# Kernel optimization log

Measured on AMD Instinct MI355X. Metric: run time of the kernel, lower is better.

Reference implementation:

```python
import jax, jax.numpy as jnp
import numpy as np

OUT, IN = 8192, 8192
GROUP = 128
N_GROUPS = IN // GROUP
BATCH = 64


def dequant_int4(packed, scales):
    # packed: [OUT, IN//2] int32 bytes in [0,256); two 4-bit codes per byte
    low = packed & 0xF            # first element of each pair
    high = (packed >> 4) & 0xF    # second element
    q = jnp.stack([low, high], axis=-1).reshape(OUT, IN)  # interleaved nibbles
    # symmetric grouped dequant: w = (q - 8) * scale, scale per [row, group]
    qg = q.reshape(OUT, N_GROUPS, GROUP).astype(scales.dtype)
    w = (qg - 8.0) * scales[:, :, None]
    return w.reshape(OUT, IN)


def setup_inputs() -> dict:
    key = jax.random.key(0)
    k1, k2, k3 = jax.random.split(key, 3)
    x = jax.random.normal(k1, (BATCH, IN), dtype=jnp.float32)
    packed = jax.random.randint(k2, (OUT, IN // 2), 0, 256, dtype=jnp.int32)
    scales = jax.random.uniform(k3, (OUT, N_GROUPS), dtype=jnp.float32)
    return {"x": x, "packed": packed, "scales": scales}


def reference(x, packed, scales):
    # Dequantize int4 weights then dense matmul (F.linear, no bias)
    w = dequant_int4(packed, scales)        # [OUT, IN]
    return jnp.einsum('bi,oi->bo', x, w)    # [BATCH, OUT]
```

## Files before the change

kernel.cpp:

```cpp
#include <hip/hip_runtime.h>
#include <hip/hip_bf16.h>
#include <stdint.h>

#define OUTN   8192
#define INN    8192
#define NGRP   64
#define BATCHN 64
#define BN     64
#define BK     64
#define KSPLIT 8
#define KCHUNK (INN / KSPLIT)
#define NITER  (KCHUNK / BK)
#define NGRPC  (KCHUNK / 128)
#define OSZ    (BATCHN * OUTN)

typedef __attribute__((ext_vector_type(8))) short bf16x8;
typedef __attribute__((ext_vector_type(8))) unsigned short u16x8;
typedef __attribute__((ext_vector_type(4))) float f32x4;
typedef __attribute__((ext_vector_type(4))) unsigned int u32x4;

__device__ __forceinline__ unsigned short f2bf(float f) {
  __hip_bfloat16 h = __float2bfloat16(f);
  return __builtin_bit_cast(unsigned short, h);
}
__device__ __forceinline__ float bf2f(unsigned short h) {
  unsigned int u = ((unsigned int)h) << 16;
  return __builtin_bit_cast(float, u);
}

__device__ __forceinline__ void gll16(const void* g, void* l) {
  __builtin_amdgcn_global_load_lds(
      (const __attribute__((address_space(1))) unsigned int*)g,
      (__attribute__((address_space(3))) unsigned int*)l, 16, 0, 0);
}

__global__ void qlin_prep(const float* __restrict__ x, float* __restrict__ xsum,
                          unsigned short* __restrict__ xbf) {
  const int b = blockIdx.x;
  const int t = threadIdx.x;
  const float* xrow = x + (size_t)b * INN + t * 32;
  unsigned short* orow = xbf + (size_t)b * INN + t * 32;
  float s = 0.0f;
#pragma unroll
  for (int c = 0; c < 4; ++c) {
    float4 v0 = *(const float4*)(xrow + c * 8);
    float4 v1 = *(const float4*)(xrow + c * 8 + 4);
    u16x8 h;
    h[0] = f2bf(v0.x); h[1] = f2bf(v0.y); h[2] = f2bf(v0.z); h[3] = f2bf(v0.w);
    h[4] = f2bf(v1.x); h[5] = f2bf(v1.y); h[6] = f2bf(v1.z); h[7] = f2bf(v1.w);
#pragma unroll
    for (int j = 0; j < 8; ++j) s += bf2f(h[j]);
    *(u16x8*)(orow + c * 8) = h;
  }
  __shared__ float parts[256];
  parts[t] = s;
  __syncthreads();
  if (t < NGRP) {
    float g = parts[4 * t] + parts[4 * t + 1] + parts[4 * t + 2] + parts[4 * t + 3];
    xsum[t * BATCHN + b] = g;
  }
}

__global__ __launch_bounds__(256, 4) void qlin_main(
    const int* __restrict__ packed, const unsigned short* __restrict__ xbf,
    const float* __restrict__ scales, const float* __restrict__ xsum,
    float* __restrict__ out, float* __restrict__ part) {
  const int bx    = blockIdx.x;
  const int ks    = bx & (KSPLIT - 1);
  const int ntile = bx >> 3;
  const int o0    = ntile * BN;
  const int g0    = ks * NGRPC;

  const int t    = threadIdx.x;
  const int lane = t & 63;
  const int w    = t >> 6;
  const int l15  = lane & 15;
  const int quad = lane >> 4;

  __shared__ __align__(16) int4  pkb[3][512];
  __shared__ __align__(16) int4  xb[3][512];
  __shared__ __align__(16) float st[BN][9];
  __shared__ __align__(16) float xs[NGRPC][BATCHN];

#pragma unroll
  for (int i = 0; i < 2; ++i) {
    int v = t * 2 + i;
    int ol = v >> 3, gl = v & 7;
    st[ol][gl] = scales[(size_t)(o0 + ol) * NGRP + g0 + gl];
    int gl2 = v >> 6, b2 = v & 63;
    xs[gl2][b2] = xsum[(g0 + gl2) * BATCHN + b2];
  }

  const int row0 = t >> 3;
  const int p0   = t & 7;
  const int c0   = p0 ^ (row0 & 7);
  const char* pk0 = (const char*)packed + (size_t)(o0 + row0) * 16384 + ks * 2048 + c0 * 16;
  const char* pk1 = pk0 + (size_t)32 * 16384;
  const char* xg0 = (const char*)xbf + (size_t)row0 * 16384 + ks * 2048 + c0 * 16;
  const char* xg1 = xg0 + (size_t)32 * 16384;

  auto issue = [&](int i, int buf) {
    const size_t off = (size_t)i * 128;
    gll16(pk0 + off, &pkb[buf][t]);
    gll16(pk1 + off, &pkb[buf][256 + t]);
    gll16(xg0 + off, &xb[buf][t]);
    gll16(xg1 + off, &xb[buf][256 + t]);
  };

  f32x4 facc[4], gacc[4];
#pragma unroll
  for (int mt = 0; mt < 4; ++mt) {
    facc[mt] = (f32x4){0.f, 0.f, 0.f, 0.f};
    gacc[mt] = (f32x4){0.f, 0.f, 0.f, 0.f};
  }

  issue(0, 0);
  issue(1, 1);

  const int browB = w * 16 + l15;
  const int sw    = l15 & 7;

#pragma unroll
  for (int i = 0; i < NITER; ++i) {
    if (i == 0)
      asm volatile("s_waitcnt vmcnt(4) lgkmcnt(0)" ::: "memory");
    else if (i == NITER - 1)
      asm volatile("s_waitcnt vmcnt(0)" ::: "memory");
    else
      asm volatile("s_waitcnt vmcnt(4)" ::: "memory");
    __builtin_amdgcn_sched_barrier(0);
    __builtin_amdgcn_s_barrier();
    __builtin_amdgcn_sched_barrier(0);

    if (i + 2 < NITER) issue(i + 2, (i + 2) % 3);

    const int cur = i % 3;
#pragma unroll
    for (int kq = 0; kq < 2; ++kq) {
      const int ch = kq * 4 + quad;
      int4 v = pkb[cur][browB * 8 + (ch ^ sw)];
      u32x4 bw;
      bw.x = 0x43004300u | ((unsigned)v.x & 0xFu) | (((unsigned)v.x & 0xF0u) << 12);
      bw.y = 0x43004300u | ((unsigned)v.y & 0xFu) | (((unsigned)v.y & 0xF0u) << 12);
      bw.z = 0x43004300u | ((unsigned)v.z & 0xFu) | (((unsigned)v.z & 0xF0u) << 12);
      bw.w = 0x43004300u | ((unsigned)v.w & 0xFu) | (((unsigned)v.w & 0xF0u) << 12);
      bf16x8 bfv = __builtin_bit_cast(bf16x8, bw);
#pragma unroll
      for (int mt = 0; mt < 4; ++mt) {
        bf16x8 af = *(const bf16x8*)&xb[cur][(mt * 16 + l15) * 8 + (ch ^ sw)];
        gacc[mt] = __builtin_amdgcn_mfma_f32_16x16x32_bf16(af, bfv, gacc[mt], 0, 0, 0);
      }
    }

    if (i & 1) {
      const int g = i >> 1;
      float s0 = st[browB][g];
#pragma unroll
      for (int mt = 0; mt < 4; ++mt) {
        f32x4 xv = *(const f32x4*)&xs[g][mt * 16 + quad * 4];
#pragma unroll
        for (int r = 0; r < 4; ++r) {
          facc[mt][r] += s0 * (gacc[mt][r] - 136.0f * xv[r]);
          gacc[mt][r] = 0.f;
        }
      }
    }
  }

  const int obase = o0 + browB;
  if (part) {
    float* pb = part + (size_t)ks * OSZ;
#pragma unroll
    for (int mt = 0; mt < 4; ++mt)
#pragma unroll
      for (int r = 0; r < 4; ++r) {
        int m = mt * 16 + quad * 4 + r;
        pb[(size_t)m * OUTN + obase] = facc[mt][r];
      }
  } else {
#pragma unroll
    for (int mt = 0; mt < 4; ++mt)
#pragma unroll
      for (int r = 0; r < 4; ++r) {
        int m = mt * 16 + quad * 4 + r;
        atomicAdd(&out[(size_t)m * OUTN + obase], facc[mt][r]);
      }
  }
}

__global__ void qlin_reduce(const float* __restrict__ part, float* __restrict__ out) {
  const size_t i = ((size_t)blockIdx.x * 256 + threadIdx.x) * 4;
  float4 s = *(const float4*)(part + i);
#pragma unroll
  for (int ks = 1; ks < KSPLIT; ++ks) {
    float4 v = *(const float4*)(part + (size_t)ks * OSZ + i);
    s.x += v.x; s.y += v.y; s.z += v.z; s.w += v.w;
  }
  *(float4*)(out + i) = s;
}

extern "C" void kernel_launch(void* const* d_in, const int* in_sizes, int n_in,
                              void* d_out, int out_size, void* d_ws, size_t ws_size,
                              hipStream_t stream) {
  const float* x      = (const float*)d_in[0];
  const int*   packed = (const int*)d_in[1];
  const float* scales = (const float*)d_in[2];
  float* out  = (float*)d_out;

  float*          xsum = (float*)d_ws;
  unsigned short* xbf  = (unsigned short*)((char*)d_ws + 16384);
  const size_t part_off = 16384 + (size_t)BATCHN * INN * 2;
  const size_t need = part_off + (size_t)KSPLIT * OSZ * sizeof(float);
  float* part = (ws_size >= need) ? (float*)((char*)d_ws + part_off) : nullptr;

  qlin_prep<<<BATCHN, 256, 0, stream>>>(x, xsum, xbf);
  if (!part)
    hipMemsetAsync(d_out, 0, (size_t)out_size * sizeof(float), stream);
  qlin_main<<<(OUTN / BN) * KSPLIT, 256, 0, stream>>>(packed, xbf, scales, xsum, out, part);
  if (part)
    qlin_reduce<<<OSZ / 4 / 256, 256, 0, stream>>>(part, out);
}
```

Baseline: 212.3 us.

## Load packed weights directly into registers instead of staging through LDS

Packed int4 weight tiles are now fetched by each lane straight from global memory into registers, double-buffered as even and odd register sets one iteration ahead. They no longer go through global_load_lds into a triple-buffered LDS array. This drops the LDS write and read traffic for weights, along with their bank-swizzle lookups, and frees 24KB of shared memory. The cost is more registers, only one iteration of prefetch distance for the weights, and vmcnt accounting that now mixes direct vector loads with the LDS-bound x loads.

```diff
diff --git a/kernel.cpp b/kernel.cpp
--- a/kernel.cpp
+++ b/kernel.cpp
@@ -77,7 +77,6 @@
   const int l15  = lane & 15;
   const int quad = lane >> 4;
 
-  __shared__ __align__(16) int4  pkb[3][512];
   __shared__ __align__(16) int4  xb[3][512];
   __shared__ __align__(16) float st[BN][9];
   __shared__ __align__(16) float xs[NGRPC][BATCHN];
@@ -91,22 +90,25 @@
     xs[gl2][b2] = xsum[(g0 + gl2) * BATCHN + b2];
   }
 
+  const int browB = w * 16 + l15;
+  const int sw    = l15 & 7;
+
   const int row0 = t >> 3;
-  const int p0   = t & 7;
-  const int c0   = p0 ^ (row0 & 7);
-  const char* pk0 = (const char*)packed + (size_t)(o0 + row0) * 16384 + ks * 2048 + c0 * 16;
-  const char* pk1 = pk0 + (size_t)32 * 16384;
+  const int c0   = (t & 7) ^ (row0 & 7);
   const char* xg0 = (const char*)xbf + (size_t)row0 * 16384 + ks * 2048 + c0 * 16;
   const char* xg1 = xg0 + (size_t)32 * 16384;
 
-  auto issue = [&](int i, int buf) {
+  auto issueG = [&](int i, int buf) {
     const size_t off = (size_t)i * 128;
-    gll16(pk0 + off, &pkb[buf][t]);
-    gll16(pk1 + off, &pkb[buf][256 + t]);
     gll16(xg0 + off, &xb[buf][t]);
     gll16(xg1 + off, &xb[buf][256 + t]);
   };
 
+  const char* pkL = (const char*)packed + (size_t)(o0 + browB) * 16384 +
+                    ks * 2048 + quad * 16;
+
+  int4 pkE[2], pkO[2];
+
   f32x4 facc[4], gacc[4];
 #pragma unroll
   for (int mt = 0; mt < 4; ++mt) {
@@ -114,31 +116,38 @@
     gacc[mt] = (f32x4){0.f, 0.f, 0.f, 0.f};
   }
 
-  issue(0, 0);
-  issue(1, 1);
-
-  const int browB = w * 16 + l15;
-  const int sw    = l15 & 7;
+  pkE[0] = *(const int4*)(pkL);
+  pkE[1] = *(const int4*)(pkL + 64);
+  __builtin_amdgcn_sched_barrier(0);
+  issueG(0, 0);
+  issueG(1, 1);
+  __builtin_amdgcn_sched_barrier(0);
 
 #pragma unroll
   for (int i = 0; i < NITER; ++i) {
     if (i == 0)
-      asm volatile("s_waitcnt vmcnt(4) lgkmcnt(0)" ::: "memory");
+      asm volatile("s_waitcnt vmcnt(2) lgkmcnt(0)" ::: "memory");
     else if (i == NITER - 1)
       asm volatile("s_waitcnt vmcnt(0)" ::: "memory");
     else
-      asm volatile("s_waitcnt vmcnt(4)" ::: "memory");
+      asm volatile("s_waitcnt vmcnt(2)" ::: "memory");
     __builtin_amdgcn_sched_barrier(0);
     __builtin_amdgcn_s_barrier();
     __builtin_amdgcn_sched_barrier(0);
 
-    if (i + 2 < NITER) issue(i + 2, (i + 2) % 3);
+    if (i + 1 < NITER) {
+      const char* p = pkL + (size_t)(i + 1) * 128;
+      if ((i + 1) & 1) { pkO[0] = *(const int4*)p; pkO[1] = *(const int4*)(p + 64); }
+      else             { pkE[0] = *(const int4*)p; pkE[1] = *(const int4*)(p + 64); }
+    }
+    if (i + 2 < NITER) issueG(i + 2, (i + 2) % 3);
+    __builtin_amdgcn_sched_barrier(0);
 
     const int cur = i % 3;
 #pragma unroll
     for (int kq = 0; kq < 2; ++kq) {
       const int ch = kq * 4 + quad;
-      int4 v = pkb[cur][browB * 8 + (ch ^ sw)];
+      int4 v = (i & 1) ? pkO[kq] : pkE[kq];
       u32x4 bw;
       bw.x = 0x43004300u | ((unsigned)v.x & 0xFu) | (((unsigned)v.x & 0xF0u) << 12);
       bw.y = 0x43004300u | ((unsigned)v.y & 0xFu) | (((unsigned)v.y & 0xF0u) << 12);
```

Result: no change. 209.3 us (-1.4%).
